# Kernel optimization log

Hardware: AMD Instinct MI355X
Metric: run time of the kernel (lower is better)

## Reference

```python
import jax, jax.numpy as jnp
import numpy as np


def gcn_conv(x, src, dst, W, b, num_nodes):
    """PyG GCNConv: out = D^{-1/2} (A+I) D^{-1/2} X W + b (self-loops already in src/dst)."""
    h = x @ W  # [N, F_out]
    ones = jnp.ones(dst.shape[0], dtype=x.dtype)
    deg = jax.ops.segment_sum(ones, dst, num_segments=num_nodes)  # in-degree incl self-loop
    dis = jnp.where(deg > 0, jax.lax.rsqrt(deg), jnp.zeros_like(deg))  # deg^{-1/2}
    norm = dis[src] * dis[dst]  # [E]
    msg = h[src] * norm[:, None]  # gather + scale, [E, F_out]
    out = jax.ops.segment_sum(msg, dst, num_segments=num_nodes) + b
    return out


def setup_inputs() -> dict:
    key = jax.random.key(0)
    k = jax.random.split(key, 6)
    N, E, F_IN, HID, C = 100000, 3200000, 128, 16, 8
    x = jax.random.normal(k[0], (N, F_IN), dtype=jnp.float32)
    edge_index = jax.random.randint(k[1], (2, E), 0, N, dtype=jnp.int64)
    W1 = jax.random.normal(k[2], (F_IN, HID), dtype=jnp.float32) * (1.0 / np.sqrt(F_IN))
    b1 = jnp.zeros((HID,), dtype=jnp.float32)
    W2 = jax.random.normal(k[3], (HID, C), dtype=jnp.float32) * (1.0 / np.sqrt(HID))
    b2 = jnp.zeros((C,), dtype=jnp.float32)
    return {"x": x, "edge_index": edge_index, "W1": W1, "b1": b1, "W2": W2, "b2": b2}


def reference(x, edge_index, W1, b1, W2, b2):
    N = x.shape[0]
    loop = jnp.arange(N, dtype=edge_index.dtype)
    src = jnp.concatenate([edge_index[0], loop])  # add self-loops
    dst = jnp.concatenate([edge_index[1], loop])
    h = gcn_conv(x, src, dst, W1, b1, N)
    h = jax.nn.relu(h)  # dropout is identity in eval mode
    out = gcn_conv(h, src, dst, W2, b2, N)
    return out
```

## Files before the change

### kernel.cpp

```cpp
#include <hip/hip_runtime.h>
#include <hip/hip_fp16.h>

#define F_IN 128
#define HID 16
#define C_OUT 8
#define BSH 6
#define BSZ 64
#define G1 1024
#define NBMAX 1600
#define CAP 3072

typedef unsigned int uint;
typedef uint ui4 __attribute__((ext_vector_type(4)));

__device__ inline int chunk_of_block(int blk) {
    return ((blk & 7) << 7) | (blk >> 3);
}

__global__ void count_kernel(const int* __restrict__ dst, uint* __restrict__ counts,
                             int E, int CE, int NB) {
    __shared__ uint h[NBMAX];
    int chunk = chunk_of_block(blockIdx.x), tid = threadIdx.x;
    for (int i = tid; i < NB; i += 256) h[i] = 0;
    __syncthreads();
    int base = chunk * CE, end = min(E, base + CE);
    int n = end - base;
    if (n > 0) {
        int n4 = n >> 2;
        const int4* p = reinterpret_cast<const int4*>(dst + base);
        for (int i = tid; i < n4; i += 256) {
            int4 d = p[i];
            atomicAdd(&h[((uint)d.x) >> BSH], 1u);
            atomicAdd(&h[((uint)d.y) >> BSH], 1u);
            atomicAdd(&h[((uint)d.z) >> BSH], 1u);
            atomicAdd(&h[((uint)d.w) >> BSH], 1u);
        }
        for (int i = base + (n4 << 2) + tid; i < end; i += 256)
            atomicAdd(&h[((uint)dst[i]) >> BSH], 1u);
    }
    __syncthreads();
    for (int i = tid; i < NB; i += 256)
        counts[(size_t)i * G1 + chunk] = h[i];
}

__global__ void scanA_kernel(uint* __restrict__ counts, uint* __restrict__ btot) {
    int b = blockIdx.x, tid = threadIdx.x;
    int lane = tid & 63, wid = tid >> 6;
    uint v = counts[(size_t)b * G1 + tid];
    uint inc = v;
#pragma unroll
    for (int o = 1; o < 64; o <<= 1) {
        uint t = __shfl_up(inc, o);
        if (lane >= o) inc += t;
    }
    __shared__ uint wsum[16];
    if (lane == 63) wsum[wid] = inc;
    __syncthreads();
    if (tid < 16) {
        uint w = wsum[tid], iw = w;
#pragma unroll
        for (int o = 1; o < 16; o <<= 1) {
            uint t = __shfl_up(iw, o);
            if (tid >= o) iw += t;
        }
        wsum[tid] = iw - w;
        if (tid == 15) btot[b] = iw;
    }
    __syncthreads();
    counts[(size_t)b * G1 + tid] = wsum[wid] + inc - v;
}

__global__ void scanB_kernel(const uint* __restrict__ btot, uint* __restrict__ bbase,
                             int NB, int E) {
    __shared__ uint wsum[4];
    __shared__ uint ctot;
    int tid = threadIdx.x, lane = tid & 63, wid = tid >> 6;
    uint base = 0;
    for (int c0 = 0; c0 < NB; c0 += 256) {
        int i = c0 + tid;
        uint v = (i < NB) ? btot[i] : 0u;
        uint inc = v;
#pragma unroll
        for (int o = 1; o < 64; o <<= 1) {
            uint t = __shfl_up(inc, o);
            if (lane >= o) inc += t;
        }
        if (lane == 63) wsum[wid] = inc;
        __syncthreads();
        if (tid == 0) {
            uint s = 0;
#pragma unroll
            for (int k = 0; k < 4; ++k) { uint t = wsum[k]; wsum[k] = s; s += t; }
            ctot = s;
        }
        __syncthreads();
        if (i < NB) bbase[i] = base + wsum[wid] + inc - v;
        base += ctot;
        __syncthreads();
    }
    if (tid == 0) bbase[NB] = (uint)E;
}

__global__ void place_kernel(const int* __restrict__ src, const int* __restrict__ dst,
                             const uint* __restrict__ offs, const uint* __restrict__ bbase,
                             uint* __restrict__ rec, int E, int CE, int NB) {
    __shared__ uint cur[NBMAX];
    int chunk = chunk_of_block(blockIdx.x), tid = threadIdx.x;
    for (int i = tid; i < NB; i += 256)
        cur[i] = bbase[i] + offs[(size_t)i * G1 + chunk];
    __syncthreads();
    int base = chunk * CE, end = min(E, base + CE);
    int n = end - base;
    if (n <= 0) return;
    int n4 = n >> 2;
    const int4* ps = reinterpret_cast<const int4*>(src + base);
    const int4* pd = reinterpret_cast<const int4*>(dst + base);
    for (int i = tid; i < n4; i += 256) {
        int4 s = ps[i];
        int4 d = pd[i];
        uint p0 = atomicAdd(&cur[((uint)d.x) >> BSH], 1u);
        rec[p0] = (uint)s.x | (((uint)d.x & (BSZ - 1)) << 17);
        uint p1 = atomicAdd(&cur[((uint)d.y) >> BSH], 1u);
        rec[p1] = (uint)s.y | (((uint)d.y & (BSZ - 1)) << 17);
        uint p2 = atomicAdd(&cur[((uint)d.z) >> BSH], 1u);
        rec[p2] = (uint)s.z | (((uint)d.z & (BSZ - 1)) << 17);
        uint p3 = atomicAdd(&cur[((uint)d.w) >> BSH], 1u);
        rec[p3] = (uint)s.w | (((uint)d.w & (BSZ - 1)) << 17);
    }
    for (int i = base + (n4 << 2) + tid; i < end; i += 256) {
        int d = dst[i];
        uint b = ((uint)d) >> BSH;
        uint p = atomicAdd(&cur[b], 1u);
        rec[p] = (uint)src[i] | (((uint)d & (BSZ - 1)) << 17);
    }
}

__global__ void sortdis_kernel(uint* __restrict__ rec, const uint* __restrict__ bbase,
                               uint* __restrict__ nstart, float* __restrict__ dis,
                               int N, int NB) {
    __shared__ uint tmp[CAP];
    __shared__ uint h[BSZ];
    __shared__ uint cur[BSZ];
    int b = blockIdx.x, tid = threadIdx.x;
    uint lane = (uint)(tid & 63);
    if (tid < BSZ) h[tid] = 0;
    uint s0 = bbase[b], s1 = bbase[b + 1];
    uint seg = min(s1 - s0, (uint)CAP);
    __syncthreads();

    uint hreg = 0;
    uint i = (uint)tid;
    uint wbase = (uint)(tid & ~63);
    while (wbase + 64 <= seg) {
        uint r = rec[s0 + i];
        tmp[i] = r;
        uint bin = (r >> 17) & 63u;
        unsigned long long bal[6];
#pragma unroll
        for (int bit = 0; bit < 6; ++bit)
            bal[bit] = __ballot((bin >> bit) & 1u);
        unsigned long long m = ~0ull;
#pragma unroll
        for (int bit = 0; bit < 6; ++bit)
            m &= ((lane >> bit) & 1u) ? bal[bit] : ~bal[bit];
        hreg += (uint)__popcll(m);
        i += 256; wbase += 256;
    }
    while (i < seg) {
        uint r = rec[s0 + i];
        tmp[i] = r;
        atomicAdd(&h[(r >> 17) & 63u], 1u);
        i += 256;
    }
    if (hreg) atomicAdd(&h[lane], hreg);
    __syncthreads();

    if (tid < BSZ) {
        uint v = h[tid], inc = v;
#pragma unroll
        for (int o = 1; o < BSZ; o <<= 1) {
            uint t = __shfl_up(inc, o);
            if (tid >= o) inc += t;
        }
        uint excl = inc - v;
        cur[tid] = s0 + excl;
        int n = b * BSZ + tid;
        if (n < N) {
            nstart[n] = s0 + excl;
            dis[n] = rsqrtf((float)v + 1.0f);
        }
    }
    if (b == NB - 1 && tid == 0) nstart[N] = s1;
    __syncthreads();

    i = (uint)tid;
    wbase = (uint)(tid & ~63);
    while (wbase + 64 <= seg) {
        uint r = tmp[i];
        uint bin = (r >> 17) & 63u;
        unsigned long long m = ~0ull;
#pragma unroll
        for (int bit = 0; bit < 6; ++bit) {
            unsigned long long bal = __ballot((bin >> bit) & 1u);
            m &= ((bin >> bit) & 1u) ? bal : ~bal;
        }
        uint leader = (uint)__ffsll((unsigned long long)m) - 1u;
        uint rank = (uint)__popcll(m & ((1ull << lane) - 1ull));
        uint basep = 0;
        if (lane == leader) basep = atomicAdd(&cur[bin], (uint)__popcll(m));
        basep = (uint)__shfl((int)basep, (int)leader);
        rec[basep + rank] = r & 0x1FFFFu;
        i += 256; wbase += 256;
    }
    while (i < seg) {
        uint r = tmp[i];
        uint p = atomicAdd(&cur[(r >> 17) & 63u], 1u);
        rec[p] = r & 0x1FFFFu;
        i += 256;
    }
}

__global__ void h1_kernel(const float* __restrict__ x, const float* __restrict__ W1,
                          const float* __restrict__ dis, __half* __restrict__ hs1, int N) {
    __shared__ float w[F_IN * HID];
    for (int t = threadIdx.x; t < F_IN * HID; t += blockDim.x) w[t] = W1[t];
    __syncthreads();
    int row = blockIdx.x * blockDim.x + threadIdx.x;
    if (row >= N) return;
    float acc[HID];
#pragma unroll
    for (int j = 0; j < HID; ++j) acc[j] = 0.f;
    const float4* xr = reinterpret_cast<const float4*>(x + (size_t)row * F_IN);
#pragma unroll 4
    for (int k4 = 0; k4 < F_IN / 4; ++k4) {
        float4 v = xr[k4];
        int k = k4 * 4;
#pragma unroll
        for (int j = 0; j < HID; ++j) {
            acc[j] += v.x * w[(k + 0) * HID + j] + v.y * w[(k + 1) * HID + j]
                    + v.z * w[(k + 2) * HID + j] + v.w * w[(k + 3) * HID + j];
        }
    }
    float d = dis[row];
    uint u[8];
#pragma unroll
    for (int p = 0; p < 8; ++p) {
        __half2 hh = __floats2half2_rn(acc[2 * p] * d, acc[2 * p + 1] * d);
        u[p] = *reinterpret_cast<uint*>(&hh);
    }
    uint4* o = reinterpret_cast<uint4*>(hs1 + ((size_t)row << 4));
    o[0] = make_uint4(u[0], u[1], u[2], u[3]);
    o[1] = make_uint4(u[4], u[5], u[6], u[7]);
}

__device__ inline void acc8(uint4 v, float* a) {
    float2 f;
    f = __half22float2(*reinterpret_cast<const __half2*>(&v.x)); a[0] += f.x; a[1] += f.y;
    f = __half22float2(*reinterpret_cast<const __half2*>(&v.y)); a[2] += f.x; a[3] += f.y;
    f = __half22float2(*reinterpret_cast<const __half2*>(&v.z)); a[4] += f.x; a[5] += f.y;
    f = __half22float2(*reinterpret_cast<const __half2*>(&v.w)); a[6] += f.x; a[7] += f.y;
}

__global__ void agg1_kernel(const uint* __restrict__ rec, const uint* __restrict__ nstart,
                            const __half* __restrict__ hs1, const float* __restrict__ dis,
                            const float* __restrict__ b1v, const float* __restrict__ W2,
                            __half* __restrict__ hs2, int N) {
    __shared__ float w2s[HID * C_OUT];
    __shared__ float b1s[HID];
    int tid = threadIdx.x;
    if (tid < HID * C_OUT) w2s[tid] = W2[tid];
    if (tid < HID) b1s[tid] = b1v[tid];
    __syncthreads();
    int ldn = tid >> 2;
    uint q  = (uint)(tid & 1);
    uint rr = (uint)((tid >> 1) & 1);
    int n = blockIdx.x * 64 + ldn;
    if (n >= N) return;
    uint e0 = nstart[n], e1 = nstart[n + 1];
    uint mid = (e0 + e1 + 1) >> 1;
    uint e  = rr ? mid : e0;
    uint en = rr ? e1 : mid;
    const uint4* hb = reinterpret_cast<const uint4*>(hs1) + q;
    float a[8];
#pragma unroll
    for (int j = 0; j < 8; ++j) a[j] = 0.f;
    while (e < en && (e & 3u)) {
        uint4 v = hb[(size_t)rec[e] << 1];
        acc8(v, a);
        ++e;
    }
    while (e + 8 <= en) {
        ui4 rA = __builtin_nontemporal_load(reinterpret_cast<const ui4*>(rec + e));
        ui4 rB = __builtin_nontemporal_load(reinterpret_cast<const ui4*>(rec + e + 4));
        uint4 v0 = hb[(size_t)rA.x << 1];
        uint4 v1 = hb[(size_t)rA.y << 1];
        uint4 v2 = hb[(size_t)rA.z << 1];
        uint4 v3 = hb[(size_t)rA.w << 1];
        uint4 v4 = hb[(size_t)rB.x << 1];
        uint4 v5 = hb[(size_t)rB.y << 1];
        uint4 v6 = hb[(size_t)rB.z << 1];
        uint4 v7 = hb[(size_t)rB.w << 1];
        acc8(v0, a); acc8(v1, a); acc8(v2, a); acc8(v3, a);
        acc8(v4, a); acc8(v5, a); acc8(v6, a); acc8(v7, a);
        e += 8;
    }
    if (e + 4 <= en) {
        ui4 rA = __builtin_nontemporal_load(reinterpret_cast<const ui4*>(rec + e));
        uint4 v0 = hb[(size_t)rA.x << 1];
        uint4 v1 = hb[(size_t)rA.y << 1];
        uint4 v2 = hb[(size_t)rA.z << 1];
        uint4 v3 = hb[(size_t)rA.w << 1];
        acc8(v0, a); acc8(v1, a); acc8(v2, a); acc8(v3, a);
        e += 4;
    }
    while (e < en) {
        uint4 v = hb[(size_t)rec[e] << 1];
        acc8(v, a);
        ++e;
    }
#pragma unroll
    for (int j = 0; j < 8; ++j) a[j] += __shfl_xor(a[j], 2);
    uint4 sv = hb[(size_t)n << 1];
    float s[8];
    {
        float2 f;
        f = __half22float2(*reinterpret_cast<const __half2*>(&sv.x)); s[0] = f.x; s[1] = f.y;
        f = __half22float2(*reinterpret_cast<const __half2*>(&sv.y)); s[2] = f.x; s[3] = f.y;
        f = __half22float2(*reinterpret_cast<const __half2*>(&sv.z)); s[4] = f.x; s[5] = f.y;
        f = __half22float2(*reinterpret_cast<const __half2*>(&sv.w)); s[6] = f.x; s[7] = f.y;
    }
    float dv = dis[n];
    float r[8];
#pragma unroll
    for (int j = 0; j < 8; ++j)
        r[j] = fmaxf(dv * (a[j] + s[j]) + b1s[q * 8 + j], 0.f);
    float p[C_OUT];
#pragma unroll
    for (int c = 0; c < C_OUT; ++c) {
        float t = 0.f;
#pragma unroll
        for (int j = 0; j < 8; ++j) t += r[j] * w2s[(q * 8 + j) * C_OUT + c];
        p[c] = t;
    }
#pragma unroll
    for (int c = 0; c < C_OUT; ++c) p[c] += __shfl_xor(p[c], 1);
    if (rr == 0) {
        __half2 hA = __floats2half2_rn(p[q * 4 + 0] * dv, p[q * 4 + 1] * dv);
        __half2 hB = __floats2half2_rn(p[q * 4 + 2] * dv, p[q * 4 + 3] * dv);
        uint2 u;
        u.x = *reinterpret_cast<uint*>(&hA);
        u.y = *reinterpret_cast<uint*>(&hB);
        *reinterpret_cast<uint2*>(hs2 + ((size_t)n << 3) + (q << 2)) = u;
    }
}

__global__ void agg2_kernel(const uint* __restrict__ rec, const uint* __restrict__ nstart,
                            const __half* __restrict__ hs2, const float* __restrict__ dis,
                            const float* __restrict__ b2v, float* __restrict__ out, int N) {
    int tid = threadIdx.x;
    int ldn = tid >> 2;
    uint rr = (uint)(tid & 3);
    int n = blockIdx.x * 64 + ldn;
    if (n >= N) return;
    uint e0 = nstart[n], e1 = nstart[n + 1];
    const uint4* hb = reinterpret_cast<const uint4*>(hs2);
    float a[8];
#pragma unroll
    for (int j = 0; j < 8; ++j) a[j] = 0.f;
    uint ea = min((e0 + 3u) & ~3u, e1);
    for (uint i = e0 + rr; i < ea; i += 4)
        acc8(hb[rec[i]], a);
    uint i = ea + (rr << 2);
    while (i + 4 <= e1) {
        ui4 r4 = __builtin_nontemporal_load(reinterpret_cast<const ui4*>(rec + i));
        uint4 v0 = hb[r4.x];
        uint4 v1 = hb[r4.y];
        uint4 v2 = hb[r4.z];
        uint4 v3 = hb[r4.w];
        acc8(v0, a); acc8(v1, a); acc8(v2, a); acc8(v3, a);
        i += 16;
    }
    uint pend = min(i + 4, e1);
    for (uint j = i; j < pend; ++j)
        acc8(hb[rec[j]], a);
#pragma unroll
    for (int j = 0; j < 8; ++j) {
        a[j] += __shfl_xor(a[j], 1);
        a[j] += __shfl_xor(a[j], 2);
    }
    if (rr < 2) {
        uint q = rr;
        uint4 sv = hb[n];
        float s[8];
        {
            float2 f;
            f = __half22float2(*reinterpret_cast<const __half2*>(&sv.x)); s[0] = f.x; s[1] = f.y;
            f = __half22float2(*reinterpret_cast<const __half2*>(&sv.y)); s[2] = f.x; s[3] = f.y;
            f = __half22float2(*reinterpret_cast<const __half2*>(&sv.z)); s[4] = f.x; s[5] = f.y;
            f = __half22float2(*reinterpret_cast<const __half2*>(&sv.w)); s[6] = f.x; s[7] = f.y;
        }
        float dv = dis[n];
        float4 o;
        o.x = dv * (a[q * 4 + 0] + s[q * 4 + 0]) + b2v[q * 4 + 0];
        o.y = dv * (a[q * 4 + 1] + s[q * 4 + 1]) + b2v[q * 4 + 1];
        o.z = dv * (a[q * 4 + 2] + s[q * 4 + 2]) + b2v[q * 4 + 2];
        o.w = dv * (a[q * 4 + 3] + s[q * 4 + 3]) + b2v[q * 4 + 3];
        *reinterpret_cast<float4*>(out + ((size_t)n << 3) + (q << 2)) = o;
    }
}

extern "C" void kernel_launch(void* const* d_in, const int* in_sizes, int n_in,
                              void* d_out, int out_size, void* d_ws, size_t ws_size,
                              hipStream_t stream) {
    const float* x  = (const float*)d_in[0];
    const int*   ei = (const int*)d_in[1];
    const float* W1 = (const float*)d_in[2];
    const float* b1 = (const float*)d_in[3];
    const float* W2 = (const float*)d_in[4];
    const float* b2 = (const float*)d_in[5];
    float* out = (float*)d_out;

    int N = in_sizes[0] / F_IN;
    int E = in_sizes[1] / 2;
    const int* src = ei;
    const int* dst = ei + E;

    int NB = (N + BSZ - 1) / BSZ;
    int CE = (((E + G1 - 1) / G1) + 3) & ~3;

    __half* hs1    = (__half*)d_ws;
    __half* hs2    = (__half*)((uint*)d_ws + (size_t)8 * N);
    float*  dis    = (float*)((uint*)d_ws + (size_t)12 * N);
    uint*   nstart = (uint*)(dis + N);
    uint*   rec    = nstart + ((N + 1 + 3) & ~3);
    uint*   counts = rec + E;
    uint*   btot   = counts + (size_t)NB * G1;
    uint*   bbase  = btot + NB;

    const int B = 256;
    count_kernel<<<G1, B, 0, stream>>>(dst, counts, E, CE, NB);
    scanA_kernel<<<NB, G1, 0, stream>>>(counts, btot);
    scanB_kernel<<<1, B, 0, stream>>>(btot, bbase, NB, E);
    place_kernel<<<G1, B, 0, stream>>>(src, dst, counts, bbase, rec, E, CE, NB);
    sortdis_kernel<<<NB, B, 0, stream>>>(rec, bbase, nstart, dis, N, NB);
    h1_kernel<<<(N + B - 1) / B, B, 0, stream>>>(x, W1, dis, hs1, N);
    agg1_kernel<<<(N + 63) / 64, B, 0, stream>>>(rec, nstart, hs1, dis, b1, W2, hs2, N);
    agg2_kernel<<<(N + 63) / 64, B, 0, stream>>>(rec, nstart, hs2, dis, b2, out, N);
}
```

Before: 142.6 us.

## Fuse X·W1 projection into per-bucket sort kernel, splitting rows across 4 lanes

Removes the separate h1 kernel and computes the first-layer projection inside the sort/degree kernel, one bucket of 64 nodes per block. Each node row is split across 4 threads that reduce partial sums with xor shuffles, and the freshly computed deg^{-1/2} is read from shared memory instead of global. This saves a kernel launch and the global round trip for dis. In exchange every sort block now also loads W1 (8 KB) into shared memory, and the larger shared footprint may lower occupancy of the sort phase.

```diff
diff --git a/kernel.cpp b/kernel.cpp
--- a/kernel.cpp
+++ b/kernel.cpp
@@ -135,15 +135,19 @@
     }
 }
 
-__global__ void sortdis_kernel(uint* __restrict__ rec, const uint* __restrict__ bbase,
-                               uint* __restrict__ nstart, float* __restrict__ dis,
-                               int N, int NB) {
+__global__ void sortdis_h1_kernel(uint* __restrict__ rec, const uint* __restrict__ bbase,
+                                  uint* __restrict__ nstart, float* __restrict__ dis,
+                                  const float* __restrict__ x, const float* __restrict__ W1,
+                                  __half* __restrict__ hs1, int N, int NB) {
     __shared__ uint tmp[CAP];
     __shared__ uint h[BSZ];
     __shared__ uint cur[BSZ];
+    __shared__ float disS[BSZ];
+    __shared__ float w1s[F_IN * HID];
     int b = blockIdx.x, tid = threadIdx.x;
     uint lane = (uint)(tid & 63);
     if (tid < BSZ) h[tid] = 0;
+    for (int i = tid; i < F_IN * HID; i += 256) w1s[i] = W1[i];
     uint s0 = bbase[b], s1 = bbase[b + 1];
     uint seg = min(s1 - s0, (uint)CAP);
     __syncthreads();
@@ -184,10 +188,12 @@
         }
         uint excl = inc - v;
         cur[tid] = s0 + excl;
+        float dv = rsqrtf((float)v + 1.0f);
+        disS[tid] = dv;
         int n = b * BSZ + tid;
         if (n < N) {
             nstart[n] = s0 + excl;
-            dis[n] = rsqrtf((float)v + 1.0f);
+            dis[n] = dv;
         }
     }
     if (b == NB - 1 && tid == 0) nstart[N] = s1;
@@ -218,39 +224,39 @@
         rec[p] = r & 0x1FFFFu;
         i += 256;
     }
-}
-
-__global__ void h1_kernel(const float* __restrict__ x, const float* __restrict__ W1,
-                          const float* __restrict__ dis, __half* __restrict__ hs1, int N) {
-    __shared__ float w[F_IN * HID];
-    for (int t = threadIdx.x; t < F_IN * HID; t += blockDim.x) w[t] = W1[t];
-    __syncthreads();
-    int row = blockIdx.x * blockDim.x + threadIdx.x;
-    if (row >= N) return;
-    float acc[HID];
-#pragma unroll
-    for (int j = 0; j < HID; ++j) acc[j] = 0.f;
-    const float4* xr = reinterpret_cast<const float4*>(x + (size_t)row * F_IN);
-#pragma unroll 4
-    for (int k4 = 0; k4 < F_IN / 4; ++k4) {
-        float4 v = xr[k4];
-        int k = k4 * 4;
-#pragma unroll
-        for (int j = 0; j < HID; ++j) {
-            acc[j] += v.x * w[(k + 0) * HID + j] + v.y * w[(k + 1) * HID + j]
-                    + v.z * w[(k + 2) * HID + j] + v.w * w[(k + 3) * HID + j];
-        }
-    }
-    float d = dis[row];
-    uint u[8];
-#pragma unroll
-    for (int p = 0; p < 8; ++p) {
-        __half2 hh = __floats2half2_rn(acc[2 * p] * d, acc[2 * p + 1] * d);
-        u[p] = *reinterpret_cast<uint*>(&hh);
-    }
-    uint4* o = reinterpret_cast<uint4*>(hs1 + ((size_t)row << 4));
-    o[0] = make_uint4(u[0], u[1], u[2], u[3]);
-    o[1] = make_uint4(u[4], u[5], u[6], u[7]);
+
+    {
+        int ldn = tid >> 2, c = tid & 3;
+        int n = b * BSZ + ldn;
+        if (n < N) {
+            float acc[HID];
+#pragma unroll
+            for (int j = 0; j < HID; ++j) acc[j] = 0.f;
+            const float4* xr = reinterpret_cast<const float4*>(x + (size_t)n * F_IN + c * 32);
+#pragma unroll
+            for (int it = 0; it < 8; ++it) {
+                float4 v = xr[it];
+                int k = c * 32 + it * 4;
+#pragma unroll
+                for (int j = 0; j < HID; ++j) {
+                    acc[j] += v.x * w1s[(k + 0) * HID + j] + v.y * w1s[(k + 1) * HID + j]
+                            + v.z * w1s[(k + 2) * HID + j] + v.w * w1s[(k + 3) * HID + j];
+                }
+            }
+#pragma unroll
+            for (int j = 0; j < HID; ++j) {
+                acc[j] += __shfl_xor(acc[j], 1);
+                acc[j] += __shfl_xor(acc[j], 2);
+            }
+            float dv = disS[ldn];
+            __half2 hA = __floats2half2_rn(acc[c * 4 + 0] * dv, acc[c * 4 + 1] * dv);
+            __half2 hB = __floats2half2_rn(acc[c * 4 + 2] * dv, acc[c * 4 + 3] * dv);
+            uint2 u;
+            u.x = *reinterpret_cast<uint*>(&hA);
+            u.y = *reinterpret_cast<uint*>(&hB);
+            *reinterpret_cast<uint2*>(hs1 + ((size_t)n << 4) + (c << 2)) = u;
+        }
+    }
 }
 
 __device__ inline void acc8(uint4 v, float* a) {
@@ -442,8 +448,7 @@
     scanA_kernel<<<NB, G1, 0, stream>>>(counts, btot);
     scanB_kernel<<<1, B, 0, stream>>>(btot, bbase, NB, E);
     place_kernel<<<G1, B, 0, stream>>>(src, dst, counts, bbase, rec, E, CE, NB);
-    sortdis_kernel<<<NB, B, 0, stream>>>(rec, bbase, nstart, dis, N, NB);
-    h1_kernel<<<(N + B - 1) / B, B, 0, stream>>>(x, W1, dis, hs1, N);
+    sortdis_h1_kernel<<<NB, B, 0, stream>>>(rec, bbase, nstart, dis, x, W1, hs1, N, NB);
     agg1_kernel<<<(N + 63) / 64, B, 0, stream>>>(rec, nstart, hs1, dis, b1, W2, hs2, N);
     agg2_kernel<<<(N + 63) / 64, B, 0, stream>>>(rec, nstart, hs2, dis, b2, out, N);
 }
```

After: 146.2 us. 2.5% more time.
